# Kernel optimization log

Hardware: AMD Instinct MI355X
Metric: run time of the kernel (lower is better)

Reference implementation:

```python
import jax, jax.numpy as jnp
import numpy as np

N = 100000
E = 1600000
GENE = 512
HID = 128
NCLS = 10
EPS = 1e-5  # BatchNorm1d default eps


def setup_inputs() -> dict:
    key = jax.random.key(0)
    ks = jax.random.split(key, 16)
    def lin(k, fan_in, fan_out):
        return (jax.random.normal(k, (fan_in, fan_out), jnp.float32) / np.sqrt(fan_in)).astype(jnp.float32)
    dims = [(GENE, HID), (HID, 2 * HID), (2 * HID, HID), (HID, HID // 2)]
    inp = {}
    inp["x"] = jax.random.normal(ks[0], (N, GENE), jnp.float32)
    inp["edge_index"] = jax.random.randint(ks[1], (2, E), 0, N)
    for i, (di, do) in enumerate(dims, start=1):
        inp[f"W{i}"] = lin(ks[1 + i], di, do)
        inp[f"b{i}"] = jnp.zeros((do,), jnp.float32)
        inp[f"g{i}"] = jnp.ones((do,), jnp.float32)     # BN gamma
        inp[f"beta{i}"] = jnp.zeros((do,), jnp.float32)  # BN beta
    inp["Wc"] = lin(ks[10], HID // 2, NCLS)
    inp["bc"] = jnp.zeros((NCLS,), jnp.float32)
    return inp


def gcn_conv(h_in, W, b, src, dst, deg_inv_sqrt):
    # PyG GCNConv: transform, then symmetric-normalized aggregation with self-loops
    h = h_in @ W                                   # [N, out]
    norm = (deg_inv_sqrt[src] * deg_inv_sqrt[dst])[:, None]  # [E, 1]
    agg = jnp.zeros_like(h).at[dst].add(h[src] * norm)       # scatter-add over edges
    agg = agg + h * (deg_inv_sqrt ** 2)[:, None]   # self-loop contribution (norm = 1/deg)
    return agg + b


def relu_bn(h, g, beta):
    # forward applies BatchNorm1d(F.relu(h)) in training mode (batch stats, biased var)
    h = jax.nn.relu(h)
    mu = h.mean(axis=0)
    var = h.var(axis=0)
    return (h - mu) * jax.lax.rsqrt(var + EPS) * g + beta


def reference(x, edge_index, W1, b1, g1, beta1, W2, b2, g2, beta2,
              W3, b3, g3, beta3, W4, b4, g4, beta4, Wc, bc):
    src, dst = edge_index[0], edge_index[1]
    # degree after adding self-loops (edge weight 1)
    deg = jnp.zeros((x.shape[0],), x.dtype).at[dst].add(1.0) + 1.0
    dis = jax.lax.rsqrt(deg)
    h = relu_bn(gcn_conv(x, W1, b1, src, dst, dis), g1, beta1)
    h = relu_bn(gcn_conv(h, W2, b2, src, dst, dis), g2, beta2)
    h = relu_bn(gcn_conv(h, W3, b3, src, dst, dis), g3, beta3)
    h = relu_bn(gcn_conv(h, W4, b4, src, dst, dis), g4, beta4)
    return h @ Wc + bc
```

## Files before the change

kernel.cpp:

```cpp
#include <hip/hip_runtime.h>
#include <hip/hip_bf16.h>

#define EPS_BN 1e-5f

using frag8 = __attribute__((ext_vector_type(8))) short;
using f32x4 = __attribute__((ext_vector_type(4))) float;

typedef const __attribute__((address_space(1))) void* gas_ptr;
typedef __attribute__((address_space(3))) void* las_ptr;

__device__ __forceinline__ void async_ld16(const void* g, void* l) {
  __builtin_amdgcn_global_load_lds((gas_ptr)g, (las_ptr)l, 16, 0, 0);
}

__device__ __forceinline__ float bfu2f(unsigned short u) {
  union { unsigned int i; float f; } c;
  c.i = (unsigned int)u << 16;
  return c.f;
}


__global__ void count_ticket_kernel(const int* __restrict__ dst, int* __restrict__ cnt,
                                    int* __restrict__ rank, int E) {
  int e = blockIdx.x * blockDim.x + threadIdx.x;
  if (e < E) rank[e] = atomicAdd(&cnt[dst[e]], 1);
}

__global__ void scan1_kernel(const int* __restrict__ cnt, int* __restrict__ out,
                             int* __restrict__ bsum, float* __restrict__ dis, int n) {
  __shared__ int sdata[1024];
  int tid = threadIdx.x;
  int i = blockIdx.x * 1024 + tid;
  int v = (i < n) ? cnt[i] : 0;
  if (i < n) dis[i] = rsqrtf((float)v + 1.0f);
  sdata[tid] = v;
  __syncthreads();
  for (int off = 1; off < 1024; off <<= 1) {
    int t = (tid >= off) ? sdata[tid - off] : 0;
    __syncthreads();
    sdata[tid] += t;
    __syncthreads();
  }
  if (i < n) out[i] = sdata[tid] - v;
  if (tid == 1023) bsum[blockIdx.x] = sdata[1023];
}

__global__ void scan2_kernel(int* __restrict__ bsum, int nb) {
  __shared__ int sdata[1024];
  int tid = threadIdx.x;
  int v = (tid < nb) ? bsum[tid] : 0;
  sdata[tid] = v;
  __syncthreads();
  for (int off = 1; off < 1024; off <<= 1) {
    int t = (tid >= off) ? sdata[tid - off] : 0;
    __syncthreads();
    sdata[tid] += t;
    __syncthreads();
  }
  if (tid < nb) bsum[tid] = sdata[tid] - v;
}

__global__ void scan3_kernel(int* __restrict__ out, const int* __restrict__ bsum,
                             int n, int E) {
  int i = blockIdx.x * 1024 + threadIdx.x;
  if (i < n) out[i] += bsum[blockIdx.x];
  if (i == 0) out[n] = E;
}

__global__ void scatter_kernel(const int* __restrict__ src, const int* __restrict__ dst,
                               const int* __restrict__ rowstart, const int* __restrict__ rank,
                               int* __restrict__ csr_src, int E) {
  int e = blockIdx.x * blockDim.x + threadIdx.x;
  if (e < E) csr_src[rowstart[dst[e]] + rank[e]] = src[e];
}


__global__ void convert_bf16_kernel(const float* __restrict__ in,
                                    __hip_bfloat16* __restrict__ out, size_t n4) {
  size_t i = (size_t)blockIdx.x * blockDim.x + threadIdx.x;
  size_t stride = (size_t)gridDim.x * blockDim.x;
  for (; i < n4; i += stride) {
    float4 v = *(const float4*)&in[i * 4];
    union { ushort4 u; __hip_bfloat16 h[4]; } pk;
    pk.h[0] = __float2bfloat16(v.x);
    pk.h[1] = __float2bfloat16(v.y);
    pk.h[2] = __float2bfloat16(v.z);
    pk.h[3] = __float2bfloat16(v.w);
    *(ushort4*)&out[i * 4] = pk.u;
  }
}

__global__ void wtrans_all_kernel(const float* __restrict__ W1, const float* __restrict__ W2,
                                  const float* __restrict__ W3, const float* __restrict__ W4,
                                  __hip_bfloat16* __restrict__ T1, __hip_bfloat16* __restrict__ T2,
                                  __hip_bfloat16* __restrict__ T3, __hip_bfloat16* __restrict__ T4) {
  int i = blockIdx.x * blockDim.x + threadIdx.x;
  const float* W; __hip_bfloat16* T; int K, F, base;
  if (i < 65536)        { W = W1; T = T1; K = 512; F = 128; base = 0; }
  else if (i < 98304)   { W = W2; T = T2; K = 128; F = 256; base = 65536; }
  else if (i < 131072)  { W = W3; T = T3; K = 256; F = 128; base = 98304; }
  else if (i < 139264)  { W = W4; T = T4; K = 128; F = 64;  base = 131072; }
  else return;
  int j = i - base;
  int k = j / F, f = j % F;
  T[f * K + k] = __float2bfloat16(W[j]);
}

template <int TN, int OMODE>
__global__ __launch_bounds__(256) void mfma_gemm_kernel(
    const __hip_bfloat16* __restrict__ A, const __hip_bfloat16* __restrict__ Bt,
    void* __restrict__ Cv, const float* __restrict__ bias,
    const float* __restrict__ rowscale, int Nr, int K, int F) {
  constexpr int WM = (TN == 128) ? 64 : 32;
  constexpr int MI = WM / 16;
  __shared__ __align__(16) __hip_bfloat16 As[128 * 32];
  __shared__ __align__(16) __hip_bfloat16 Bs[TN * 32];
  int tid = (int)threadIdx.x;
  int wid = tid >> 6, lane = tid & 63;
  int rowBase = blockIdx.x * 128;
  int colBase = blockIdx.y * TN;
  int wr, wc;
  if (TN == 128) { wr = (wid >> 1) * 64; wc = (wid & 1) * 64; }
  else           { wr = wid * 32;        wc = 0; }

  f32x4 zero = {0.f, 0.f, 0.f, 0.f};
  f32x4 acc[MI][4];
#pragma unroll
  for (int i = 0; i < MI; ++i)
#pragma unroll
    for (int j = 0; j < 4; ++j) acc[i][j] = zero;

  int lm = lane & 15;
  int k8 = (lane >> 4) * 8;

  for (int k0 = 0; k0 < K; k0 += 32) {
#pragma unroll
    for (int p = 0; p < 2; ++p) {
      int sidx = p * 256 + tid;
      int row = sidx >> 2;
      int kq = (sidx & 3) * 8;
      int gr = rowBase + row;
      if (gr >= Nr) gr = Nr - 1;
      async_ld16(A + (size_t)gr * K + k0 + kq, (char*)As + (p * 256 + wid * 64) * 16);
    }
    constexpr int BPASS = TN / 64;
#pragma unroll
    for (int p = 0; p < BPASS; ++p) {
      int sidx = p * 256 + tid;
      int col = sidx >> 2;
      int kq = (sidx & 3) * 8;
      async_ld16(Bt + (size_t)(colBase + col) * K + k0 + kq,
                 (char*)Bs + (p * 256 + wid * 64) * 16);
    }
    __syncthreads();

    frag8 af[MI], bf[4];
#pragma unroll
    for (int i = 0; i < MI; ++i)
      af[i] = *(const frag8*)&As[(wr + i * 16 + lm) * 32 + k8];
#pragma unroll
    for (int j = 0; j < 4; ++j)
      bf[j] = *(const frag8*)&Bs[(wc + j * 16 + lm) * 32 + k8];
#pragma unroll
    for (int i = 0; i < MI; ++i)
#pragma unroll
      for (int j = 0; j < 4; ++j)
        acc[i][j] = __builtin_amdgcn_mfma_f32_16x16x32_bf16(af[i], bf[j], acc[i][j], 0, 0, 0);
    __syncthreads();
  }

  int rquad = (lane >> 4) * 4;
#pragma unroll
  for (int i = 0; i < MI; ++i) {
    int rb = rowBase + wr + i * 16 + rquad;
#pragma unroll
    for (int r = 0; r < 4; ++r) {
      int row = rb + r;
      if (row < Nr) {
        if constexpr (OMODE == 1) {
          float rs = rowscale[row];
#pragma unroll
          for (int j = 0; j < 4; ++j) {
            int col = colBase + wc + j * 16 + lm;
            ((__hip_bfloat16*)Cv)[(size_t)row * F + col] = __float2bfloat16(acc[i][j][r] * rs);
          }
        } else {
#pragma unroll
          for (int j = 0; j < 4; ++j) {
            int col = colBase + wc + j * 16 + lm;
            ((float*)Cv)[(size_t)row * F + col] = acc[i][j][r] + bias[col];
          }
        }
      }
    }
  }
}

template <int VEC, bool BF16OUT>
__global__ __launch_bounds__(256) void agg_kernel(
    const __hip_bfloat16* __restrict__ Ts, const int* __restrict__ rowstart,
    const int* __restrict__ csr_src, const float* __restrict__ dis,
    const float* __restrict__ bias, void* __restrict__ H, int Nn, int F) {
  int gt = blockIdx.x * blockDim.x + (int)threadIdx.x;
  int wid = gt >> 6;
  int lane = (int)threadIdx.x & 63;
  if (wid >= Nn) return;
  int d = wid;
  int off = lane * VEC;
  const unsigned short* Tu = (const unsigned short*)Ts;

  float acc[VEC];
  {
    unsigned short r[VEC];
    if constexpr (VEC == 2) *(ushort2*)r = *(const ushort2*)&Tu[(size_t)d * F + off];
    else                    r[0] = Tu[(size_t)d * F + off];
#pragma unroll
    for (int j = 0; j < VEC; ++j) acc[j] = bfu2f(r[j]);
  }

  int e0 = rowstart[d], e1 = rowstart[d + 1];
  int e = e0;
  for (; e + 8 <= e1; e += 8) {
    int s[8];
#pragma unroll
    for (int q = 0; q < 8; ++q) s[q] = csr_src[e + q];
    unsigned short r[8][VEC];
#pragma unroll
    for (int q = 0; q < 8; ++q) {
      if constexpr (VEC == 2) *(ushort2*)r[q] = *(const ushort2*)&Tu[(size_t)s[q] * F + off];
      else                    r[q][0] = Tu[(size_t)s[q] * F + off];
    }
#pragma unroll
    for (int q = 0; q < 8; ++q)
#pragma unroll
      for (int j = 0; j < VEC; ++j) acc[j] += bfu2f(r[q][j]);
  }
  for (; e < e1; ++e) {
    int s = csr_src[e];
    unsigned short r[VEC];
    if constexpr (VEC == 2) *(ushort2*)r = *(const ushort2*)&Tu[(size_t)s * F + off];
    else                    r[0] = Tu[(size_t)s * F + off];
#pragma unroll
    for (int j = 0; j < VEC; ++j) acc[j] += bfu2f(r[j]);
  }

  float dd = dis[d];
  if constexpr (BF16OUT) {
#pragma unroll
    for (int j = 0; j < VEC; ++j)
      ((__hip_bfloat16*)H)[(size_t)d * F + off + j] = __float2bfloat16(acc[j] * dd);
  } else {
#pragma unroll
    for (int j = 0; j < VEC; ++j)
      ((float*)H)[(size_t)d * F + off + j] = acc[j] * dd + bias[off + j];
  }
}

__global__ __launch_bounds__(256) void stat_kernel(const float* __restrict__ H,
                                                   float* __restrict__ stats, int Nn, int F) {
  int tid = (int)threadIdx.x;
  int c = tid & (F - 1);
  int rg = tid / F;
  int RP = 256 / F;
  float s = 0.f, sq = 0.f;
  for (int r = blockIdx.x * RP + rg; r < Nn; r += gridDim.x * RP) {
    float v = H[(size_t)r * F + c];
    v = fmaxf(v, 0.f);
    s += v;
    sq += v * v;
  }
  __shared__ float ls[256], lq[256];
  ls[tid] = s; lq[tid] = sq;
  __syncthreads();
  for (int str = 128; str >= F; str >>= 1) {
    if (tid < str) { ls[tid] += ls[tid + str]; lq[tid] += lq[tid + str]; }
    __syncthreads();
  }
  if (tid < F) {
    atomicAdd(&stats[c], ls[tid]);
    atomicAdd(&stats[256 + c], lq[tid]);
  }
}

__global__ void bnfin_kernel(float* __restrict__ stats, const float* __restrict__ g,
                             const float* __restrict__ beta, float* __restrict__ ss,
                             int Nn, int F) {
  int c = (int)threadIdx.x;
  if (c < F) {
    float mean = stats[c] / (float)Nn;
    float var = stats[256 + c] / (float)Nn - mean * mean;
    float sc = g[c] * rsqrtf(var + EPS_BN);
    ss[c] = sc;
    ss[256 + c] = beta[c] - mean * sc;
  }
  stats[c] = 0.f;
  stats[256 + c] = 0.f;
}

__global__ void bnapply_kernel(const float* __restrict__ H, const float* __restrict__ ss,
                               const float* __restrict__ rowscale,
                               __hip_bfloat16* __restrict__ O, size_t total4, int F, int logF) {
  size_t i = (size_t)blockIdx.x * blockDim.x + threadIdx.x;
  size_t stride = (size_t)gridDim.x * blockDim.x;
  for (; i < total4; i += stride) {
    size_t b = i * 4;
    float4 v = *(const float4*)&H[b];
    int c = (int)(b & (size_t)(F - 1));
    float rs = rowscale ? rowscale[b >> logF] : 1.0f;
    union { ushort4 u; __hip_bfloat16 h[4]; } pk;
    pk.h[0] = __float2bfloat16((fmaxf(v.x, 0.f) * ss[c + 0] + ss[256 + c + 0]) * rs);
    pk.h[1] = __float2bfloat16((fmaxf(v.y, 0.f) * ss[c + 1] + ss[256 + c + 1]) * rs);
    pk.h[2] = __float2bfloat16((fmaxf(v.z, 0.f) * ss[c + 2] + ss[256 + c + 2]) * rs);
    pk.h[3] = __float2bfloat16((fmaxf(v.w, 0.f) * ss[c + 3] + ss[256 + c + 3]) * rs);
    *(ushort4*)&O[b] = pk.u;
  }
}

__global__ __launch_bounds__(256) void cls_kernel(const __hip_bfloat16* __restrict__ H,
                                                  const float* __restrict__ Wc,
                                                  const float* __restrict__ bc,
                                                  float* __restrict__ out, int Nn) {
  int gt = blockIdx.x * blockDim.x + (int)threadIdx.x;
  int wid = gt >> 6;
  int lane = (int)threadIdx.x & 63;
  if (wid >= Nn) return;
  float v = __bfloat162float(H[(size_t)wid * 64 + lane]);
#pragma unroll
  for (int c = 0; c < 10; ++c) {
    float p = v * Wc[lane * 10 + c];
#pragma unroll
    for (int off = 32; off > 0; off >>= 1) p += __shfl_down(p, off, 64);
    if (lane == 0) out[(size_t)wid * 10 + c] = p + bc[c];
  }
}


extern "C" void kernel_launch(void* const* d_in, const int* in_sizes, int n_in,
                              void* d_out, int out_size, void* d_ws, size_t ws_size,
                              hipStream_t stream) {
  (void)n_in; (void)out_size; (void)ws_size;
  const float* x    = (const float*)d_in[0];
  const int*   edge = (const int*)d_in[1];
  const int E  = in_sizes[1] / 2;
  const int Nn = in_sizes[0] / 512;
  const int* e_src = edge;
  const int* e_dst = edge + E;

  const float* W[4]  = {(const float*)d_in[2],  (const float*)d_in[6],
                        (const float*)d_in[10], (const float*)d_in[14]};
  const float* bv[4] = {(const float*)d_in[3],  (const float*)d_in[7],
                        (const float*)d_in[11], (const float*)d_in[15]};
  const float* gv[4] = {(const float*)d_in[4],  (const float*)d_in[8],
                        (const float*)d_in[12], (const float*)d_in[16]};
  const float* bt[4] = {(const float*)d_in[5],  (const float*)d_in[9],
                        (const float*)d_in[13], (const float*)d_in[17]};
  const float* Wc = (const float*)d_in[18];
  const float* bc = (const float*)d_in[19];
  float* out = (float*)d_out;

  const int Kdim[4] = {512, 128, 256, 128};
  const int Fdim[4] = {128, 256, 128, 64};

  char* p = (char*)d_ws;
  auto alloc = [&](size_t bytes) -> void* {
    void* r = (void*)p;
    p += (bytes + 255) & ~(size_t)255;
    return r;
  };
  int*   cnt      = (int*)alloc((size_t)Nn * 4);
  int*   rowstart = (int*)alloc((size_t)(Nn + 1) * 4);
  int*   bsum     = (int*)alloc(1024 * 4);
  float* dis      = (float*)alloc((size_t)Nn * 4);
  float* stats    = (float*)alloc(512 * 4);
  float* ss       = (float*)alloc(512 * 4);
  int*   rank     = (int*)alloc((size_t)E * 4);
  int*   csr_src  = (int*)alloc((size_t)E * 4);
  __hip_bfloat16* Wt[4];
  for (int l = 0; l < 4; ++l)
    Wt[l] = (__hip_bfloat16*)alloc((size_t)Kdim[l] * Fdim[l] * 2);
  char* R0 = (char*)alloc((size_t)Nn * 512 * 2);
  __hip_bfloat16* Tb = (__hip_bfloat16*)alloc((size_t)Nn * 256 * 2);
  __hip_bfloat16* P0 = (__hip_bfloat16*)alloc((size_t)Nn * 256 * 2);
  __hip_bfloat16* P1 = (__hip_bfloat16*)alloc((size_t)Nn * 256 * 2);
  __hip_bfloat16* Xb = (__hip_bfloat16*)R0;
  float*          Hf = (float*)R0;

  hipMemsetAsync(cnt, 0, (size_t)Nn * 4, stream);
  hipMemsetAsync(stats, 0, 512 * 4, stream);

  int nb = (Nn + 1023) / 1024;
  count_ticket_kernel<<<(E + 255) / 256, 256, 0, stream>>>(e_dst, cnt, rank, E);
  scan1_kernel<<<nb, 1024, 0, stream>>>(cnt, rowstart, bsum, dis, Nn);
  scan2_kernel<<<1, 1024, 0, stream>>>(bsum, nb);
  scan3_kernel<<<nb, 1024, 0, stream>>>(rowstart, bsum, Nn, E);
  scatter_kernel<<<(E + 255) / 256, 256, 0, stream>>>(e_src, e_dst, rowstart, rank,
                                                      csr_src, E);

  wtrans_all_kernel<<<(139264 + 255) / 256, 256, 0, stream>>>(W[0], W[1], W[2], W[3],
                                                              Wt[0], Wt[1], Wt[2], Wt[3]);
  convert_bf16_kernel<<<4096, 256, 0, stream>>>(x, Xb, (size_t)Nn * 512 / 4);

  int aggBlocks = (Nn * 64 + 255) / 256;

  auto bn = [&](const float* Hsrc, int l, int F, __hip_bfloat16* Obf, const float* rsc) {
    stat_kernel<<<1024, 256, 0, stream>>>(Hsrc, stats, Nn, F);
    bnfin_kernel<<<1, 256, 0, stream>>>(stats, gv[l], bt[l], ss, Nn, F);
    size_t total4 = (size_t)Nn * F / 4;
    int logF = (F == 256) ? 8 : (F == 128 ? 7 : 6);
    bnapply_kernel<<<(int)((total4 + 255) / 256), 256, 0, stream>>>(Hsrc, ss, rsc, Obf,
                                                                    total4, F, logF);
  };

  {
    dim3 g((Nn + 127) / 128, 1);
    mfma_gemm_kernel<128, 1><<<g, 256, 0, stream>>>(Xb, Wt[0], Tb, nullptr, dis, Nn, 512, 128);
    agg_kernel<2, false><<<aggBlocks, 256, 0, stream>>>(Tb, rowstart, csr_src, dis,
                                                        bv[0], Hf, Nn, 128);
    bn(Hf, 0, 128, P0, dis);
  }
  {
    agg_kernel<2, true><<<aggBlocks, 256, 0, stream>>>(P0, rowstart, csr_src, dis,
                                                       nullptr, Tb, Nn, 128);
    dim3 g((Nn + 127) / 128, 2);
    mfma_gemm_kernel<128, 2><<<g, 256, 0, stream>>>(Tb, Wt[1], Hf, bv[1], nullptr, Nn, 128, 256);
    bn(Hf, 1, 256, P1, nullptr);
  }
  {
    dim3 g((Nn + 127) / 128, 1);
    mfma_gemm_kernel<128, 1><<<g, 256, 0, stream>>>(P1, Wt[2], Tb, nullptr, dis, Nn, 256, 128);
    agg_kernel<2, false><<<aggBlocks, 256, 0, stream>>>(Tb, rowstart, csr_src, dis,
                                                        bv[2], Hf, Nn, 128);
    bn(Hf, 2, 128, P0, nullptr);
  }
  {
    dim3 g((Nn + 127) / 128, 1);
    mfma_gemm_kernel<64, 1><<<g, 256, 0, stream>>>(P0, Wt[3], Tb, nullptr, dis, Nn, 128, 64);
    agg_kernel<1, false><<<aggBlocks, 256, 0, stream>>>(Tb, rowstart, csr_src, dis,
                                                        bv[3], Hf, Nn, 64);
    bn(Hf, 3, 64, P1, nullptr);
  }

  int clsBlocks = (Nn * 64 + 255) / 256;
  cls_kernel<<<clsBlocks, 256, 0, stream>>>(P1, Wc, bc, out, Nn);
}
```

Baseline: 1.144 ms.

## Fuse BatchNorm statistics into GEMM/aggregation epilogues and BN-apply into classifier

```diff
diff --git a/kernel.cpp b/kernel.cpp
--- a/kernel.cpp
+++ b/kernel.cpp
@@ -110,11 +110,13 @@
 __global__ __launch_bounds__(256) void mfma_gemm_kernel(
     const __hip_bfloat16* __restrict__ A, const __hip_bfloat16* __restrict__ Bt,
     void* __restrict__ Cv, const float* __restrict__ bias,
-    const float* __restrict__ rowscale, int Nr, int K, int F) {
+    const float* __restrict__ rowscale, float* __restrict__ stats,
+    int Nr, int K, int F) {
   constexpr int WM = (TN == 128) ? 64 : 32;
   constexpr int MI = WM / 16;
   __shared__ __align__(16) __hip_bfloat16 As[128 * 32];
   __shared__ __align__(16) __hip_bfloat16 Bs[TN * 32];
+  __shared__ float sacc[128], sqc[128];
   int tid = (int)threadIdx.x;
   int wid = tid >> 6, lane = tid & 63;
   int rowBase = blockIdx.x * 128;
@@ -133,6 +135,10 @@
   int lm = lane & 15;
   int k8 = (lane >> 4) * 8;
 
+  if constexpr (OMODE == 2) {
+    if (tid < 128) { sacc[tid] = 0.f; sqc[tid] = 0.f; }
+  }
+
   for (int k0 = 0; k0 < K; k0 += 32) {
 #pragma unroll
     for (int p = 0; p < 2; ++p) {
@@ -170,6 +176,7 @@
   }
 
   int rquad = (lane >> 4) * 4;
+  float s[4] = {0.f, 0.f, 0.f, 0.f}, q[4] = {0.f, 0.f, 0.f, 0.f};
 #pragma unroll
   for (int i = 0; i < MI; ++i) {
     int rb = rowBase + wr + i * 16 + rquad;
@@ -188,97 +195,132 @@
 #pragma unroll
           for (int j = 0; j < 4; ++j) {
             int col = colBase + wc + j * 16 + lm;
-            ((float*)Cv)[(size_t)row * F + col] = acc[i][j][r] + bias[col];
+            float v = acc[i][j][r] + bias[col];
+            ((float*)Cv)[(size_t)row * F + col] = v;
+            float rl = fmaxf(v, 0.f);
+            s[j] += rl;
+            q[j] += rl * rl;
           }
         }
       }
     }
   }
-}
-
-template <int VEC, bool BF16OUT>
+
+  if constexpr (OMODE == 2) {
+#pragma unroll
+    for (int j = 0; j < 4; ++j) {
+      s[j] += __shfl_xor(s[j], 16, 64); s[j] += __shfl_xor(s[j], 32, 64);
+      q[j] += __shfl_xor(q[j], 16, 64); q[j] += __shfl_xor(q[j], 32, 64);
+    }
+    if (lane < 16) {
+#pragma unroll
+      for (int j = 0; j < 4; ++j) {
+        atomicAdd(&sacc[wc + j * 16 + lane], s[j]);
+        atomicAdd(&sqc[wc + j * 16 + lane], q[j]);
+      }
+    }
+    __syncthreads();
+    if (tid < 128) {
+      atomicAdd(&stats[colBase + tid], sacc[tid]);
+      atomicAdd(&stats[256 + colBase + tid], sqc[tid]);
+    }
+  }
+}
+
+template <int VEC, int OMODE>
 __global__ __launch_bounds__(256) void agg_kernel(
     const __hip_bfloat16* __restrict__ Ts, const int* __restrict__ rowstart,
     const int* __restrict__ csr_src, const float* __restrict__ dis,
-    const float* __restrict__ bias, void* __restrict__ H, int Nn, int F) {
-  int gt = blockIdx.x * blockDim.x + (int)threadIdx.x;
-  int wid = gt >> 6;
-  int lane = (int)threadIdx.x & 63;
-  if (wid >= Nn) return;
-  int d = wid;
+    const float* __restrict__ bias, void* __restrict__ H,
+    float* __restrict__ stats, int Nn, int F) {
+  __shared__ float lsum[512], lqs[512];
+  int tid = (int)threadIdx.x;
+  int wid4 = tid >> 6;
+  int lane = tid & 63;
   int off = lane * VEC;
   const unsigned short* Tu = (const unsigned short*)Ts;
 
-  float acc[VEC];
-  {
-    unsigned short r[VEC];
-    if constexpr (VEC == 2) *(ushort2*)r = *(const ushort2*)&Tu[(size_t)d * F + off];
-    else                    r[0] = Tu[(size_t)d * F + off];
-#pragma unroll
-    for (int j = 0; j < VEC; ++j) acc[j] = bfu2f(r[j]);
-  }
-
-  int e0 = rowstart[d], e1 = rowstart[d + 1];
-  int e = e0;
-  for (; e + 8 <= e1; e += 8) {
-    int s[8];
-#pragma unroll
-    for (int q = 0; q < 8; ++q) s[q] = csr_src[e + q];
-    unsigned short r[8][VEC];
-#pragma unroll
-    for (int q = 0; q < 8; ++q) {
-      if constexpr (VEC == 2) *(ushort2*)r[q] = *(const ushort2*)&Tu[(size_t)s[q] * F + off];
-      else                    r[q][0] = Tu[(size_t)s[q] * F + off];
-    }
-#pragma unroll
-    for (int q = 0; q < 8; ++q)
-#pragma unroll
-      for (int j = 0; j < VEC; ++j) acc[j] += bfu2f(r[q][j]);
-  }
-  for (; e < e1; ++e) {
-    int s = csr_src[e];
-    unsigned short r[VEC];
-    if constexpr (VEC == 2) *(ushort2*)r = *(const ushort2*)&Tu[(size_t)s * F + off];
-    else                    r[0] = Tu[(size_t)s * F + off];
-#pragma unroll
-    for (int j = 0; j < VEC; ++j) acc[j] += bfu2f(r[j]);
-  }
-
-  float dd = dis[d];
-  if constexpr (BF16OUT) {
-#pragma unroll
-    for (int j = 0; j < VEC; ++j)
-      ((__hip_bfloat16*)H)[(size_t)d * F + off + j] = __float2bfloat16(acc[j] * dd);
-  } else {
-#pragma unroll
-    for (int j = 0; j < VEC; ++j)
-      ((float*)H)[(size_t)d * F + off + j] = acc[j] * dd + bias[off + j];
-  }
-}
-
-__global__ __launch_bounds__(256) void stat_kernel(const float* __restrict__ H,
-                                                   float* __restrict__ stats, int Nn, int F) {
-  int tid = (int)threadIdx.x;
-  int c = tid & (F - 1);
-  int rg = tid / F;
-  int RP = 256 / F;
-  float s = 0.f, sq = 0.f;
-  for (int r = blockIdx.x * RP + rg; r < Nn; r += gridDim.x * RP) {
-    float v = H[(size_t)r * F + c];
-    v = fmaxf(v, 0.f);
-    s += v;
-    sq += v * v;
-  }
-  __shared__ float ls[256], lq[256];
-  ls[tid] = s; lq[tid] = sq;
-  __syncthreads();
-  for (int str = 128; str >= F; str >>= 1) {
-    if (tid < str) { ls[tid] += ls[tid + str]; lq[tid] += lq[tid + str]; }
-    __syncthreads();
-  }
-  if (tid < F) {
-    atomicAdd(&stats[c], ls[tid]);
-    atomicAdd(&stats[256 + c], lq[tid]);
+  float bj[VEC];
+  float s[VEC], q[VEC];
+#pragma unroll
+  for (int j = 0; j < VEC; ++j) {
+    bj[j] = (OMODE == 1) ? bias[off + j] : 0.f;
+    s[j] = 0.f; q[j] = 0.f;
+  }
+
+  for (int d = blockIdx.x * 4 + wid4; d < Nn; d += gridDim.x * 4) {
+    float acc[VEC];
+    {
+      unsigned short r[VEC];
+      if constexpr (VEC == 2) *(ushort2*)r = *(const ushort2*)&Tu[(size_t)d * F + off];
+      else                    r[0] = Tu[(size_t)d * F + off];
+#pragma unroll
+      for (int j = 0; j < VEC; ++j) acc[j] = bfu2f(r[j]);
+    }
+
+    int e0 = rowstart[d], e1 = rowstart[d + 1];
+    for (int e = e0; e < e1; e += 8) {
+      int idx[8];
+      bool val[8];
+#pragma unroll
+      for (int p = 0; p < 8; ++p) {
+        int ee = e + p;
+        val[p] = ee < e1;
+        idx[p] = csr_src[val[p] ? ee : e1 - 1];
+      }
+      unsigned short r[8][VEC];
+#pragma unroll
+      for (int p = 0; p < 8; ++p) {
+        if constexpr (VEC == 2) *(ushort2*)r[p] = *(const ushort2*)&Tu[(size_t)idx[p] * F + off];
+        else                    r[p][0] = Tu[(size_t)idx[p] * F + off];
+      }
+#pragma unroll
+      for (int p = 0; p < 8; ++p)
+#pragma unroll
+        for (int j = 0; j < VEC; ++j) acc[j] += val[p] ? bfu2f(r[p][j]) : 0.f;
+    }
+
+    float dd = dis[d];
+    if constexpr (OMODE == 0) {
+      union { ushort2 u; __hip_bfloat16 h[2]; } pk;
+      if constexpr (VEC == 2) {
+        pk.h[0] = __float2bfloat16(acc[0] * dd);
+        pk.h[1] = __float2bfloat16(acc[1] * dd);
+        *(ushort2*)&((__hip_bfloat16*)H)[(size_t)d * F + off] = pk.u;
+      } else {
+        ((__hip_bfloat16*)H)[(size_t)d * F + off] = __float2bfloat16(acc[0] * dd);
+      }
+    } else {
+      float v[VEC];
+#pragma unroll
+      for (int j = 0; j < VEC; ++j) {
+        v[j] = acc[j] * dd + bj[j];
+        float rl = fmaxf(v[j], 0.f);
+        s[j] += rl;
+        q[j] += rl * rl;
+      }
+      if constexpr (VEC == 2) {
+        *(float2*)&((float*)H)[(size_t)d * F + off] = make_float2(v[0], v[1]);
+      } else {
+        ((float*)H)[(size_t)d * F + off] = v[0];
+      }
+    }
+  }
+
+  if constexpr (OMODE == 1) {
+#pragma unroll
+    for (int j = 0; j < VEC; ++j) {
+      lsum[(lane * VEC + j) * 4 + wid4] = s[j];
+      lqs[(lane * VEC + j) * 4 + wid4] = q[j];
+    }
+    __syncthreads();
+    int nc = 64 * VEC;
+    for (int c = tid; c < nc; c += 256) {
+      float a = lsum[c * 4 + 0] + lsum[c * 4 + 1] + lsum[c * 4 + 2] + lsum[c * 4 + 3];
+      float b = lqs[c * 4 + 0] + lqs[c * 4 + 1] + lqs[c * 4 + 2] + lqs[c * 4 + 3];
+      atomicAdd(&stats[c], a);
+      atomicAdd(&stats[256 + c], b);
+    }
   }
 }
 
@@ -316,18 +358,19 @@
   }
 }
 
-__global__ __launch_bounds__(256) void cls_kernel(const __hip_bfloat16* __restrict__ H,
-                                                  const float* __restrict__ Wc,
-                                                  const float* __restrict__ bc,
-                                                  float* __restrict__ out, int Nn) {
+__global__ __launch_bounds__(256) void bnapply_cls_kernel(
+    const float* __restrict__ Hf, const float* __restrict__ ss,
+    const float* __restrict__ Wc, const float* __restrict__ bc,
+    float* __restrict__ out, int Nn) {
   int gt = blockIdx.x * blockDim.x + (int)threadIdx.x;
   int wid = gt >> 6;
   int lane = (int)threadIdx.x & 63;
   if (wid >= Nn) return;
-  float v = __bfloat162float(H[(size_t)wid * 64 + lane]);
+  float v = Hf[(size_t)wid * 64 + lane];
+  float h = fmaxf(v, 0.f) * ss[lane] + ss[256 + lane];
 #pragma unroll
   for (int c = 0; c < 10; ++c) {
-    float p = v * Wc[lane * 10 + c];
+    float p = h * Wc[lane * 10 + c];
 #pragma unroll
     for (int off = 32; off > 0; off >>= 1) p += __shfl_down(p, off, 64);
     if (lane == 0) out[(size_t)wid * 10 + c] = p + bc[c];
@@ -400,46 +443,48 @@
                                                               Wt[0], Wt[1], Wt[2], Wt[3]);
   convert_bf16_kernel<<<4096, 256, 0, stream>>>(x, Xb, (size_t)Nn * 512 / 4);
 
-  int aggBlocks = (Nn * 64 + 255) / 256;
-
-  auto bn = [&](const float* Hsrc, int l, int F, __hip_bfloat16* Obf, const float* rsc) {
-    stat_kernel<<<1024, 256, 0, stream>>>(Hsrc, stats, Nn, F);
+  const int AGG_BLOCKS = 1536;
+
+  auto bnapply = [&](int l, int F, __hip_bfloat16* Obf, const float* rsc) {
     bnfin_kernel<<<1, 256, 0, stream>>>(stats, gv[l], bt[l], ss, Nn, F);
     size_t total4 = (size_t)Nn * F / 4;
     int logF = (F == 256) ? 8 : (F == 128 ? 7 : 6);
-    bnapply_kernel<<<(int)((total4 + 255) / 256), 256, 0, stream>>>(Hsrc, ss, rsc, Obf,
+    bnapply_kernel<<<(int)((total4 + 255) / 256), 256, 0, stream>>>(Hf, ss, rsc, Obf,
                                                                     total4, F, logF);
   };
 
   {
     dim3 g((Nn + 127) / 128, 1);
-    mfma_gemm_kernel<128, 1><<<g, 256, 0, stream>>>(Xb, Wt[0], Tb, nullptr, dis, Nn, 512, 128);
-    agg_kernel<2, false><<<aggBlocks, 256, 0, stream>>>(Tb, rowstart, csr_src, dis,
-                                                        bv[0], Hf, Nn, 128);
-    bn(Hf, 0, 128, P0, dis);
+    mfma_gemm_kernel<128, 1><<<g, 256, 0, stream>>>(Xb, Wt[0], Tb, nullptr, dis, nullptr,
+                                                    Nn, 512, 128);
+    agg_kernel<2, 1><<<AGG_BLOCKS, 256, 0, stream>>>(Tb, rowstart, csr_src, dis,
+                                                     bv[0], Hf, stats, Nn, 128);
+    bnapply(0, 128, P0, dis);
   }
   {
-    agg_kernel<2, true><<<aggBlocks, 256, 0, stream>>>(P0, rowstart, csr_src, dis,
-                                                       nullptr, Tb, Nn, 128);
+    agg_kernel<2, 0><<<AGG_BLOCKS, 256, 0, stream>>>(P0, rowstart, csr_src, dis,
+                                                     nullptr, Tb, nullptr, Nn, 128);
     dim3 g((Nn + 127) / 128, 2);
-    mfma_gemm_kernel<128, 2><<<g, 256, 0, stream>>>(Tb, Wt[1], Hf, bv[1], nullptr, Nn, 128, 256);
-    bn(Hf, 1, 256, P1, nullptr);
+    mfma_gemm_kernel<128, 2><<<g, 256, 0, stream>>>(Tb, Wt[1], Hf, bv[1], nullptr, stats,
+                                                    Nn, 128, 256);
+    bnapply(1, 256, P1, nullptr);
   }
   {
     dim3 g((Nn + 127) / 128, 1);
-    mfma_gemm_kernel<128, 1><<<g, 256, 0, stream>>>(P1, Wt[2], Tb, nullptr, dis, Nn, 256, 128);
-    agg_kernel<2, false><<<aggBlocks, 256, 0, stream>>>(Tb, rowstart, csr_src, dis,
-                                                        bv[2], Hf, Nn, 128);
-    bn(Hf, 2, 128, P0, nullptr);
+    mfma_gemm_kernel<128, 1><<<g, 256, 0, stream>>>(P1, Wt[2], Tb, nullptr, dis, nullptr,
+                                                    Nn, 256, 128);
+    agg_kernel<2, 1><<<AGG_BLOCKS, 256, 0, stream>>>(Tb, rowstart, csr_src, dis,
+                                                     bv[2], Hf, stats, Nn, 128);
+    bnapply(2, 128, P0, nullptr);
   }
   {
     dim3 g((Nn + 127) / 128, 1);
-    mfma_gemm_kernel<64, 1><<<g, 256, 0, stream>>>(P0, Wt[3], Tb, nullptr, dis, Nn, 128, 64);
-    agg_kernel<1, false><<<aggBlocks, 256, 0, stream>>>(Tb, rowstart, csr_src, dis,
-                                                        bv[3], Hf, Nn, 64);
-    bn(Hf, 3, 64, P1, nullptr);
-  }
-
-  int clsBlocks = (Nn * 64 + 255) / 256;
-  cls_kernel<<<clsBlocks, 256, 0, stream>>>(P1, Wc, bc, out, Nn);
-}
+    mfma_gemm_kernel<64, 1><<<g, 256, 0, stream>>>(P0, Wt[3], Tb, nullptr, dis, nullptr,
+                                                   Nn, 128, 64);
+    agg_kernel<1, 1><<<AGG_BLOCKS, 256, 0, stream>>>(Tb, rowstart, csr_src, dis,
+                                                     bv[3], Hf, stats, Nn, 64);
+    bnfin_kernel<<<1, 256, 0, stream>>>(stats, gv[3], bt[3], ss, Nn, 64);
+    int clsBlocks = (Nn * 64 + 255) / 256;
+    bnapply_cls_kernel<<<clsBlocks, 256, 0, stream>>>(Hf, ss, Wc, bc, out, Nn);
+  }
+}
```

After: 1.044 ms. 8.7% less time.
